# Optimization experiments

Hardware: AMD Instinct MI355X
Metric: run time of the kernel (lower is better)

## Reference

```python
import jax, jax.numpy as jnp
import numpy as np

N_HEAD = 16
ROPE_BASE = 10000.0


def _rope_cos_sin(T, D, dtype):
    # inv_freq over even dims, freqs concatenated twice (rotate_half convention)
    inv_freq = 1.0 / (ROPE_BASE ** (jnp.arange(0, D, 2, dtype=jnp.float32) / D))
    t = jnp.arange(T, dtype=jnp.float32)
    freqs = jnp.outer(t, inv_freq)          # [T, D/2]
    emb = jnp.concatenate([freqs, freqs], axis=-1)  # [T, D]
    return jnp.cos(emb).astype(dtype), jnp.sin(emb).astype(dtype)


def _rotate_half(x):
    x1, x2 = jnp.split(x, 2, axis=-1)
    return jnp.concatenate([-x2, x1], axis=-1)


def setup_inputs() -> dict:
    key = jax.random.key(0)
    ks = jax.random.split(key, 5)
    B, T, C = 2, 2048, 1024
    s = 1.0 / np.sqrt(C)
    return {
        "x": jax.random.normal(ks[0], (B, T, C), jnp.float32),
        "W_attn": jax.random.normal(ks[1], (C, 3 * C), jnp.float32) * s,
        "b_attn": jax.random.normal(ks[2], (3 * C,), jnp.float32) * 0.02,
        "W_proj": jax.random.normal(ks[3], (C, C), jnp.float32) * s,
        "b_proj": jax.random.normal(ks[4], (C,), jnp.float32) * 0.02,
    }


def reference(x, W_attn, b_attn, W_proj, b_proj):
    B, T, C = x.shape
    H = N_HEAD
    D = C // H

    # fused QKV projection
    qkv = x @ W_attn + b_attn                      # [B, T, 3C]
    q, k, v = jnp.split(qkv, 3, axis=-1)
    q = q.reshape(B, T, H, D).transpose(0, 2, 1, 3)  # [B, H, T, D]
    k = k.reshape(B, T, H, D).transpose(0, 2, 1, 3)
    v = v.reshape(B, T, H, D).transpose(0, 2, 1, 3)

    # RoPE (no past_kv: applied to full q and k)
    cos, sin = _rope_cos_sin(T, D, x.dtype)        # [T, D]
    cos = cos[None, None]                          # [1, 1, T, D]
    sin = sin[None, None]
    q = q * cos + _rotate_half(q) * sin
    k = k * cos + _rotate_half(k) * sin

    # causal SDPA (dropout_p = 0 in reference)
    scale = 1.0 / np.sqrt(D)
    scores = jnp.einsum("bhqd,bhkd->bhqk", q, k) * scale
    causal = jnp.tril(jnp.ones((T, T), dtype=bool))
    scores = jnp.where(causal, scores, jnp.finfo(scores.dtype).min)
    attn = jax.nn.softmax(scores, axis=-1)
    y = jnp.einsum("bhqk,bhkd->bhqd", attn, v)     # [B, H, T, D]

    y = y.transpose(0, 2, 1, 3).reshape(B, T, C)
    y = y @ W_proj + b_proj
    return y
```

## Files before the change

kernel.cpp:

```cpp
#include <hip/hip_runtime.h>
#include <cstdint>
#include <cstddef>

#define SEQ_T 2048
#define NHEAD 16

typedef __attribute__((ext_vector_type(8))) short short8;
typedef __attribute__((ext_vector_type(4))) float f32x4;
typedef __attribute__((ext_vector_type(16))) float f32x16;

__device__ __forceinline__ unsigned short f2bf(float f) {
  union { float f; unsigned int u; } v; v.f = f;
  return (unsigned short)((v.u + 0x7FFFu + ((v.u >> 16) & 1u)) >> 16);
}

__device__ __forceinline__ unsigned cvtpk(float lo, float hi) {
  unsigned r;
  asm("v_cvt_pk_bf16_f32 %0, %1, %2" : "=v"(r) : "v"(lo), "v"(hi));
  return r;
}

#if __has_builtin(__builtin_amdgcn_permlane32_swap)
__device__ __forceinline__ void plswap(unsigned& a, unsigned& b) {
  auto r = __builtin_amdgcn_permlane32_swap(a, b, false, false);
  a = r[0];
  b = r[1];
}
#else
__device__ __forceinline__ void plswap(unsigned& a, unsigned& b) {
  asm volatile("s_nop 1\n\tv_permlane32_swap_b32 %0, %1\n\ts_nop 1"
               : "+v"(a), "+v"(b));
}
#endif

__device__ __forceinline__ float xhalf_max(float x) {
  unsigned a = __builtin_bit_cast(unsigned, x), b = a;
  plswap(a, b);
  return fmaxf(__builtin_bit_cast(float, a), __builtin_bit_cast(float, b));
}
__device__ __forceinline__ float xhalf_add(float x) {
  unsigned a = __builtin_bit_cast(unsigned, x), b = a;
  plswap(a, b);
  return __builtin_bit_cast(float, a) + __builtin_bit_cast(float, b);
}

__device__ __forceinline__ float vmax16(const f32x16 v) {
  float a0 = fmaxf(v[0], v[8]),  a1 = fmaxf(v[1], v[9]);
  float a2 = fmaxf(v[2], v[10]), a3 = fmaxf(v[3], v[11]);
  float a4 = fmaxf(v[4], v[12]), a5 = fmaxf(v[5], v[13]);
  float a6 = fmaxf(v[6], v[14]), a7 = fmaxf(v[7], v[15]);
  float b0 = fmaxf(a0, a4), b1 = fmaxf(a1, a5);
  float b2 = fmaxf(a2, a6), b3 = fmaxf(a3, a7);
  return fmaxf(fmaxf(b0, b1), fmaxf(b2, b3));
}

__device__ __forceinline__ void gl_lds16(const void* g, void* l) {
  __builtin_amdgcn_global_load_lds(
      (__attribute__((address_space(1))) void*)(void*)g,
      (__attribute__((address_space(3))) void*)l, 16, 0, 0);
}

__global__ void k_cvt(const float* __restrict__ in, unsigned short* __restrict__ out, int n4) {
  int i = blockIdx.x * 256 + threadIdx.x;
  if (i >= n4) return;
  float4 v = ((const float4*)in)[i];
  unsigned long long pk = (unsigned long long)f2bf(v.x)
                        | ((unsigned long long)f2bf(v.y) << 16)
                        | ((unsigned long long)f2bf(v.z) << 32)
                        | ((unsigned long long)f2bf(v.w) << 48);
  ((unsigned long long*)out)[i] = pk;
}

__global__ void k_tr(const float* __restrict__ in, unsigned short* __restrict__ out, int K, int N) {
  int idx = blockIdx.x * 256 + threadIdx.x;
  int n = idx % N;
  int k0 = (idx / N) * 8;
  short8 v;
#pragma unroll
  for (int j = 0; j < 8; ++j)
    v[j] = (short)f2bf(in[(size_t)(k0 + j) * N + n]);
  *(short8*)&out[(size_t)n * K + k0] = v;
}

__global__ void k_tab(float2* __restrict__ tab) {
  int idx = blockIdx.x * 256 + threadIdx.x;
  int t = idx >> 5, i = idx & 31;
  float inv = powf(10000.0f, -(float)(2 * i) / 64.0f);
  float f = (float)t * inv;
  tab[idx] = make_float2(cosf(f), sinf(f));
}

__global__ void k_gemm_qkv(const unsigned short* __restrict__ A,
                           const unsigned short* __restrict__ Bt,
                           const float* __restrict__ bias,
                           const float2* __restrict__ cs,
                           unsigned short* __restrict__ qo,
                           unsigned short* __restrict__ ko,
                           unsigned short* __restrict__ vo) {
  __shared__ unsigned short lA[128 * 32];
  __shared__ unsigned short lB[128 * 32];
  const int K = 1024;
  const int bn = blockIdx.x, bm = blockIdx.y;
  const int tid = threadIdx.x, w = tid >> 6, l = tid & 63;
  const int lr = l & 15, lh = l >> 4;
  const int wm = w >> 1, wn = w & 1;

  f32x4 acc[4][4];
#pragma unroll
  for (int m = 0; m < 4; ++m)
#pragma unroll
    for (int n = 0; n < 4; ++n)
#pragma unroll
      for (int i = 0; i < 4; ++i) acc[m][n][i] = 0.f;

  const unsigned short* ga0 = A + (size_t)(bm * 128 + w * 16 + (l >> 2)) * K + (l & 3) * 8;
  const unsigned short* gb0 = Bt + (size_t)(bn * 128 + w * 16 + (l >> 2)) * K + (l & 3) * 8;
  unsigned short* la0 = &lA[w * 512];
  unsigned short* la1 = &lA[(w + 4) * 512];
  unsigned short* lb0 = &lB[w * 512];
  unsigned short* lb1 = &lB[(w + 4) * 512];

  for (int kt = 0; kt < K; kt += 32) {
    gl_lds16(ga0 + kt, la0);
    gl_lds16(ga0 + (size_t)64 * K + kt, la1);
    gl_lds16(gb0 + kt, lb0);
    gl_lds16(gb0 + (size_t)64 * K + kt, lb1);
    __syncthreads();
    short8 af[4], bf[4];
#pragma unroll
    for (int m = 0; m < 4; ++m) af[m] = *(const short8*)&lA[(wm * 64 + m * 16 + lr) * 32 + lh * 8];
#pragma unroll
    for (int n = 0; n < 4; ++n) bf[n] = *(const short8*)&lB[(wn * 64 + n * 16 + lr) * 32 + lh * 8];
#pragma unroll
    for (int m = 0; m < 4; ++m)
#pragma unroll
      for (int n = 0; n < 4; ++n)
        acc[m][n] = __builtin_amdgcn_mfma_f32_16x16x32_bf16(af[m], bf[n], acc[m][n], 0, 0, 0);
    __syncthreads();
  }

  const int col0 = bn * 128 + wn * 64;
  const int row0 = bm * 128 + wm * 64;
  const int sec = col0 >> 10;
  const int hh = (col0 >> 6) & 15;
  float bl[4];
#pragma unroll
  for (int n = 0; n < 4; ++n) bl[n] = bias[col0 + n * 16 + lr];

  if (sec == 2) {
    const int b = row0 >> 11;
    unsigned short* vtp = vo + (size_t)(b * 16 + hh) * 64 * 2048;
#pragma unroll
    for (int n = 0; n < 4; ++n) {
      int d = n * 16 + lr;
#pragma unroll
      for (int m = 0; m < 4; ++m) {
        int t = (row0 + m * 16 + lh * 4) & 2047;
        unsigned long long pk = (unsigned long long)f2bf(acc[m][n][0] + bl[n])
                              | ((unsigned long long)f2bf(acc[m][n][1] + bl[n]) << 16)
                              | ((unsigned long long)f2bf(acc[m][n][2] + bl[n]) << 32)
                              | ((unsigned long long)f2bf(acc[m][n][3] + bl[n]) << 48);
        *(unsigned long long*)&vtp[(size_t)d * 2048 + t] = pk;
      }
    }
  } else {
    unsigned short* dst = (sec == 0) ? qo : ko;
#pragma unroll
    for (int m = 0; m < 4; ++m)
#pragma unroll
      for (int i = 0; i < 4; ++i) {
        int row = row0 + m * 16 + lh * 4 + i;
        int t = row & 2047, b = row >> 11;
        size_t ob = ((size_t)(b * 16 + hh) * 2048 + t) * 64;
#pragma unroll
        for (int n = 0; n < 4; ++n) {
          float v = acc[m][n][i] + bl[n];
          float pv = acc[m][n ^ 2][i] + bl[n ^ 2];
          int d = n * 16 + lr;
          float2 c = cs[t * 32 + (d & 31)];
          float rot = (d < 32) ? -pv : pv;
          dst[ob + d] = f2bf(v * c.x + rot * c.y);
        }
      }
  }
}

__global__ __launch_bounds__(512, 4) void k_attn(const unsigned short* __restrict__ Q,
                       const unsigned short* __restrict__ Kg,
                       const unsigned short* __restrict__ VT,
                       unsigned short* __restrict__ O) {
  __shared__ unsigned short kl[2][128 * 64];
  __shared__ unsigned short vl[2][64 * 128];
  const int id = blockIdx.x;
  const int xcd = id & 7, u = id >> 3;
  const int g = u >> 4;
  const int bh = xcd * 4 + g;
  const int s = (u + g * 4) & 15;
  const int qt = (s & 1) ? 15 - (s >> 1) : (s >> 1);
  const int tid = threadIdx.x, w = tid >> 6, l = tid & 63;
  const int wq = w & 3, wk = w >> 2;
  const int lq = l & 31, hi = l >> 5;
  const size_t base = (size_t)bh * SEQ_T * 64;
  const float CE = 0.18033688f;
  const float DTHR = 44.3614f;

  const int qrow = qt * 128 + wq * 32 + lq;
  short8 qf[4];
#pragma unroll
  for (int c = 0; c < 4; ++c)
    qf[c] = *(const short8*)&Q[base + (size_t)qrow * 64 + c * 16 + hi * 8];

  const int kv0 = tid >> 3;
  const unsigned short* ks0 = Kg + base + (size_t)kv0 * 64 + (((tid & 7) ^ (kv0 & 7)) * 8);
  const int dv0 = tid >> 4;
  const unsigned short* vs0 = VT + base + (size_t)dv0 * 2048 + (((tid & 15) ^ (dv0 & 15)) * 8);

#define STAGE(KT, BSEL) do { \
    const unsigned short* kp_ = ks0 + (size_t)(KT) * 8192; \
    const unsigned short* vp_ = vs0 + (size_t)(KT) * 128;  \
    unsigned short* kd_ = &kl[BSEL][w * 512]; \
    unsigned short* vd_ = &vl[BSEL][w * 512]; \
    gl_lds16(kp_,         kd_);        gl_lds16(kp_ + 4096,  kd_ + 4096); \
    gl_lds16(vp_,         vd_);        gl_lds16(vp_ + 65536, vd_ + 4096); \
  } while (0)

  float mi = -1.0e30f, li = 0.f;
  f32x16 oc0, oc1;
#pragma unroll
  for (int r = 0; r < 16; ++r) { oc0[r] = 0.f; oc1[r] = 0.f; }

  const int nkt = qt + 1;
  STAGE(0, 0);
  __syncthreads();

  for (int kt = 0; kt < nkt; ++kt) {
    const int cur = kt & 1;
    if (kt + 1 < nkt) STAGE(kt + 1, cur ^ 1);
    const unsigned short* kb = &kl[cur][0];
    const unsigned short* vb = &vl[cur][0];

    f32x16 st[2];
#pragma unroll
    for (int tt = 0; tt < 2; ++tt)
#pragma unroll
      for (int r = 0; r < 16; ++r) st[tt][r] = 0.f;

    __builtin_amdgcn_s_setprio(1);
#pragma unroll
    for (int tt = 0; tt < 2; ++tt) {
      const int rowb = (wk * 64 + tt * 32 + lq) * 64;
#pragma unroll
      for (int c = 0; c < 4; ++c) {
        const short8 kf = *(const short8*)&kb[rowb + (((c * 2 + hi) ^ (lq & 7)) * 8)];
        st[tt] = __builtin_amdgcn_mfma_f32_32x32x16_bf16(kf, qf[c], st[tt], 0, 0, 0);
      }
    }
    __builtin_amdgcn_s_setprio(0);

    if (kt == nkt - 1) {
#pragma unroll
      for (int tt = 0; tt < 2; ++tt)
#pragma unroll
        for (int r = 0; r < 16; ++r) {
          int kvg = kt * 128 + wk * 64 + tt * 32 + (r & 3) + 8 * (r >> 2) + 4 * hi;
          if (kvg > qrow) st[tt][r] = -3.0e38f;
        }
    }

    float tm = xhalf_max(fmaxf(vmax16(st[0]), vmax16(st[1])));

    if (!__all(tm <= mi + DTHR)) {
      float mn = fmaxf(mi, tm);
      float scq = exp2f((mi - mn) * CE);
      mi = mn;
      li *= scq;
#pragma unroll
      for (int r = 0; r < 16; ++r) {
        float sc_r = __shfl(scq, (r & 3) + 8 * (r >> 2) + 4 * hi, 64);
        oc0[r] *= sc_r;
        oc1[r] *= sc_r;
      }
    }

    const float nb = mi * CE;
    float rs = 0.f;
#pragma unroll
    for (int tt = 0; tt < 2; ++tt)
#pragma unroll
      for (int r = 0; r < 16; ++r) {
        float p = exp2f(fmaf(st[tt][r], CE, -nb));
        st[tt][r] = p;
        rs += p;
      }
    li += xhalf_add(rs);

    short8 pa[4];
#pragma unroll
    for (int kc = 0; kc < 4; ++kc) {
      const int tt = kc >> 1, o = (kc & 1) * 8;
      unsigned w0 = cvtpk(st[tt][o + 0], st[tt][o + 1]);
      unsigned w1 = cvtpk(st[tt][o + 2], st[tt][o + 3]);
      unsigned w2 = cvtpk(st[tt][o + 4], st[tt][o + 5]);
      unsigned w3 = cvtpk(st[tt][o + 6], st[tt][o + 7]);
      plswap(w0, w2);
      plswap(w1, w3);
      uint4 F;
      F.x = w0; F.y = w1; F.z = w2; F.w = w3;
      pa[kc] = __builtin_bit_cast(short8, F);
    }

    __builtin_amdgcn_s_setprio(1);
#pragma unroll
    for (int kc = 0; kc < 4; ++kc) {
      const int chs = ((wk * 8 + kc * 2 + hi) ^ (lq & 15)) * 8;
      const short8 vb0 = *(const short8*)&vb[lq * 128 + chs];
      oc0 = __builtin_amdgcn_mfma_f32_32x32x16_bf16(pa[kc], vb0, oc0, 0, 0, 0);
      const short8 vb1 = *(const short8*)&vb[(32 + lq) * 128 + chs];
      oc1 = __builtin_amdgcn_mfma_f32_32x32x16_bf16(pa[kc], vb1, oc1, 0, 0, 0);
    }
    __builtin_amdgcn_s_setprio(0);

    if (kt + 1 < nkt) __syncthreads();
  }

  __syncthreads();
  float* obuf = (float*)&kl[0][0];
  float* mlb  = (float*)&vl[0][0];
  if (wk == 1) {
#pragma unroll
    for (int r = 0; r < 16; ++r) {
      const int q = (r & 3) + 8 * (r >> 2) + 4 * hi;
      obuf[wq * 2048 + q * 64 + lq]      = oc0[r];
      obuf[wq * 2048 + q * 64 + 32 + lq] = oc1[r];
    }
    if (hi == 0) {
      mlb[wq * 64 + lq * 2 + 0] = mi;
      mlb[wq * 64 + lq * 2 + 1] = li;
    }
  }
  __syncthreads();
  if (wk == 0) {
    const int hh = bh & 15, bb = bh >> 4;
#pragma unroll
    for (int r = 0; r < 16; ++r) {
      const int q = (r & 3) + 8 * (r >> 2) + 4 * hi;
      float m0 = __shfl(mi, q, 64), l0 = __shfl(li, q, 64);
      float m1 = mlb[wq * 64 + q * 2 + 0], l1 = mlb[wq * 64 + q * 2 + 1];
      float mm = fmaxf(m0, m1);
      float f0 = exp2f((m0 - mm) * CE), f1 = exp2f((m1 - mm) * CE);
      float inv = 1.0f / (f0 * l0 + f1 * l1);
      float o0 = (f0 * oc0[r] + f1 * obuf[wq * 2048 + q * 64 + lq]) * inv;
      float o1 = (f0 * oc1[r] + f1 * obuf[wq * 2048 + q * 64 + 32 + lq]) * inv;
      int qg = qt * 128 + wq * 32 + q;
      size_t ob = (size_t)(bb * 2048 + qg) * 1024 + hh * 64;
      O[ob + lq]      = f2bf(o0);
      O[ob + 32 + lq] = f2bf(o1);
    }
  }
#undef STAGE
}

__global__ void k_gemm_proj(const unsigned short* __restrict__ A,
                            const unsigned short* __restrict__ Bt,
                            const float* __restrict__ bias,
                            float* __restrict__ out) {
  __shared__ unsigned short lA[128 * 32];
  __shared__ unsigned short lB[128 * 32];
  const int K = 1024;
  const int bn = blockIdx.x, bm = blockIdx.y;
  const int tid = threadIdx.x, w = tid >> 6, l = tid & 63;
  const int lr = l & 15, lh = l >> 4;
  const int wm = w >> 1, wn = w & 1;

  f32x4 acc[4][4];
#pragma unroll
  for (int m = 0; m < 4; ++m)
#pragma unroll
    for (int n = 0; n < 4; ++n)
#pragma unroll
      for (int i = 0; i < 4; ++i) acc[m][n][i] = 0.f;

  const unsigned short* ga0 = A + (size_t)(bm * 128 + w * 16 + (l >> 2)) * K + (l & 3) * 8;
  const unsigned short* gb0 = Bt + (size_t)(bn * 128 + w * 16 + (l >> 2)) * K + (l & 3) * 8;
  unsigned short* la0 = &lA[w * 512];
  unsigned short* la1 = &lA[(w + 4) * 512];
  unsigned short* lb0 = &lB[w * 512];
  unsigned short* lb1 = &lB[(w + 4) * 512];

  for (int kt = 0; kt < K; kt += 32) {
    gl_lds16(ga0 + kt, la0);
    gl_lds16(ga0 + (size_t)64 * K + kt, la1);
    gl_lds16(gb0 + kt, lb0);
    gl_lds16(gb0 + (size_t)64 * K + kt, lb1);
    __syncthreads();
    short8 af[4], bf[4];
#pragma unroll
    for (int m = 0; m < 4; ++m) af[m] = *(const short8*)&lA[(wm * 64 + m * 16 + lr) * 32 + lh * 8];
#pragma unroll
    for (int n = 0; n < 4; ++n) bf[n] = *(const short8*)&lB[(wn * 64 + n * 16 + lr) * 32 + lh * 8];
#pragma unroll
    for (int m = 0; m < 4; ++m)
#pragma unroll
      for (int n = 0; n < 4; ++n)
        acc[m][n] = __builtin_amdgcn_mfma_f32_16x16x32_bf16(af[m], bf[n], acc[m][n], 0, 0, 0);
    __syncthreads();
  }

  const int col0 = bn * 128 + wn * 64;
  const int row0 = bm * 128 + wm * 64;
  float bl[4];
#pragma unroll
  for (int n = 0; n < 4; ++n) bl[n] = bias[col0 + n * 16 + lr];
#pragma unroll
  for (int m = 0; m < 4; ++m)
#pragma unroll
    for (int i = 0; i < 4; ++i) {
      int row = row0 + m * 16 + lh * 4 + i;
#pragma unroll
      for (int n = 0; n < 4; ++n)
        out[(size_t)row * 1024 + col0 + n * 16 + lr] = acc[m][n][i] + bl[n];
    }
}

extern "C" void kernel_launch(void* const* d_in, const int* in_sizes, int n_in,
                              void* d_out, int out_size, void* d_ws, size_t ws_size,
                              hipStream_t stream) {
  const float* x     = (const float*)d_in[0];
  const float* Wattn = (const float*)d_in[1];
  const float* battn = (const float*)d_in[2];
  const float* Wproj = (const float*)d_in[3];
  const float* bproj = (const float*)d_in[4];
  float* out = (float*)d_out;

  char* ws = (char*)d_ws;
  unsigned short* xb  = (unsigned short*)(ws);
  unsigned short* wat = (unsigned short*)(ws + (8ull  << 20));
  unsigned short* wpt = (unsigned short*)(ws + (14ull << 20));
  unsigned short* qa  = (unsigned short*)(ws + (16ull << 20));
  unsigned short* ka  = (unsigned short*)(ws + (24ull << 20));
  unsigned short* va  = (unsigned short*)(ws + (32ull << 20));
  unsigned short* ob  = (unsigned short*)(ws + (40ull << 20));
  float2* cs          = (float2*)(ws + (48ull << 20));

  k_cvt<<<(4096 * 1024 / 4) / 256, 256, 0, stream>>>(x, xb, 4096 * 1024 / 4);
  k_tr<<<(3072 * 1024 / 8) / 256, 256, 0, stream>>>(Wattn, wat, 1024, 3072);
  k_tr<<<(1024 * 1024 / 8) / 256, 256, 0, stream>>>(Wproj, wpt, 1024, 1024);
  k_tab<<<(2048 * 32) / 256, 256, 0, stream>>>(cs);
  k_gemm_qkv<<<dim3(24, 32), 256, 0, stream>>>(xb, wat, battn, cs, qa, ka, va);
  k_attn<<<512, 512, 0, stream>>>(qa, ka, va, ob);
  k_gemm_proj<<<dim3(8, 32), 256, 0, stream>>>(ob, wpt, bproj, out);
}
```

Measured before the change: 138.8 us.

## Merge prep kernels and software-pipeline attention with 64-wide KV tiles

Folds the four preparation kernels (x conversion, two weight transposes, RoPE table) into a single launch with block-range dispatch, which removes three kernel launch gaps. The attention kernel moves from 128-wide double-buffered KV tiles to 64-wide triple-buffered tiles. QK^T for the next tile is computed before the softmax and PV of the current tile, so MFMA work overlaps with the exp and reduction work. The smaller tiles halve LDS use but double the number of loop iterations and barriers.

```diff
diff --git a/kernel.cpp b/kernel.cpp
--- a/kernel.cpp
+++ b/kernel.cpp
@@ -60,34 +60,45 @@
       (__attribute__((address_space(3))) void*)l, 16, 0, 0);
 }
 
-__global__ void k_cvt(const float* __restrict__ in, unsigned short* __restrict__ out, int n4) {
-  int i = blockIdx.x * 256 + threadIdx.x;
-  if (i >= n4) return;
-  float4 v = ((const float4*)in)[i];
-  unsigned long long pk = (unsigned long long)f2bf(v.x)
-                        | ((unsigned long long)f2bf(v.y) << 16)
-                        | ((unsigned long long)f2bf(v.z) << 32)
-                        | ((unsigned long long)f2bf(v.w) << 48);
-  ((unsigned long long*)out)[i] = pk;
-}
-
-__global__ void k_tr(const float* __restrict__ in, unsigned short* __restrict__ out, int K, int N) {
-  int idx = blockIdx.x * 256 + threadIdx.x;
-  int n = idx % N;
-  int k0 = (idx / N) * 8;
-  short8 v;
-#pragma unroll
-  for (int j = 0; j < 8; ++j)
-    v[j] = (short)f2bf(in[(size_t)(k0 + j) * N + n]);
-  *(short8*)&out[(size_t)n * K + k0] = v;
-}
-
-__global__ void k_tab(float2* __restrict__ tab) {
-  int idx = blockIdx.x * 256 + threadIdx.x;
-  int t = idx >> 5, i = idx & 31;
-  float inv = powf(10000.0f, -(float)(2 * i) / 64.0f);
-  float f = (float)t * inv;
-  tab[idx] = make_float2(cosf(f), sinf(f));
+__global__ void k_prep(const float* __restrict__ x,
+                       const float* __restrict__ Wa,
+                       const float* __restrict__ Wp,
+                       unsigned short* __restrict__ xb,
+                       unsigned short* __restrict__ wat,
+                       unsigned short* __restrict__ wpt,
+                       float2* __restrict__ tab) {
+  const int b = blockIdx.x, tid = threadIdx.x;
+  if (b < 4096) {
+    int i = b * 256 + tid;
+    float4 v = ((const float4*)x)[i];
+    unsigned long long pk = (unsigned long long)f2bf(v.x)
+                          | ((unsigned long long)f2bf(v.y) << 16)
+                          | ((unsigned long long)f2bf(v.z) << 32)
+                          | ((unsigned long long)f2bf(v.w) << 48);
+    ((unsigned long long*)xb)[i] = pk;
+  } else if (b < 5632) {
+    int idx = (b - 4096) * 256 + tid;
+    int n = idx % 3072, k0 = (idx / 3072) * 8;
+    short8 v;
+#pragma unroll
+    for (int j = 0; j < 8; ++j)
+      v[j] = (short)f2bf(Wa[(size_t)(k0 + j) * 3072 + n]);
+    *(short8*)&wat[(size_t)n * 1024 + k0] = v;
+  } else if (b < 6144) {
+    int idx = (b - 5632) * 256 + tid;
+    int n = idx & 1023, k0 = (idx >> 10) * 8;
+    short8 v;
+#pragma unroll
+    for (int j = 0; j < 8; ++j)
+      v[j] = (short)f2bf(Wp[(size_t)(k0 + j) * 1024 + n]);
+    *(short8*)&wpt[(size_t)n * 1024 + k0] = v;
+  } else {
+    int idx = (b - 6144) * 256 + tid;
+    int t = idx >> 5, i = idx & 31;
+    float inv = powf(10000.0f, -(float)(2 * i) / 64.0f);
+    float f = (float)t * inv;
+    tab[idx] = make_float2(cosf(f), sinf(f));
+  }
 }
 
 __global__ void k_gemm_qkv(const unsigned short* __restrict__ A,
@@ -189,8 +200,8 @@
                        const unsigned short* __restrict__ Kg,
                        const unsigned short* __restrict__ VT,
                        unsigned short* __restrict__ O) {
-  __shared__ unsigned short kl[2][128 * 64];
-  __shared__ unsigned short vl[2][64 * 128];
+  __shared__ unsigned short kl[3][64 * 64];
+  __shared__ unsigned short vl[3][64 * 64];
   const int id = blockIdx.x;
   const int xcd = id & 7, u = id >> 3;
   const int g = u >> 4;
@@ -210,65 +221,53 @@
   for (int c = 0; c < 4; ++c)
     qf[c] = *(const short8*)&Q[base + (size_t)qrow * 64 + c * 16 + hi * 8];
 
-  const int kv0 = tid >> 3;
-  const unsigned short* ks0 = Kg + base + (size_t)kv0 * 64 + (((tid & 7) ^ (kv0 & 7)) * 8);
-  const int dv0 = tid >> 4;
-  const unsigned short* vs0 = VT + base + (size_t)dv0 * 2048 + (((tid & 15) ^ (dv0 & 15)) * 8);
-
-#define STAGE(KT, BSEL) do { \
-    const unsigned short* kp_ = ks0 + (size_t)(KT) * 8192; \
-    const unsigned short* vp_ = vs0 + (size_t)(KT) * 128;  \
-    unsigned short* kd_ = &kl[BSEL][w * 512]; \
-    unsigned short* vd_ = &vl[BSEL][w * 512]; \
-    gl_lds16(kp_,         kd_);        gl_lds16(kp_ + 4096,  kd_ + 4096); \
-    gl_lds16(vp_,         vd_);        gl_lds16(vp_ + 65536, vd_ + 4096); \
+  const int r0 = tid >> 3, c8 = tid & 7;
+  const unsigned short* ks0 = Kg + base + (size_t)r0 * 64 + ((c8 ^ (r0 & 7)) * 8);
+  const unsigned short* vs0 = VT + base + (size_t)r0 * 2048 + ((c8 ^ (r0 & 7)) * 8);
+
+#define STAGE(KT, B) do { \
+    gl_lds16(ks0 + (size_t)(KT) * 4096, &kl[B][w * 512]); \
+    gl_lds16(vs0 + (size_t)(KT) * 64,   &vl[B][w * 512]); \
   } while (0)
 
+#define QKSTEP(KB, ST) do { \
+    const unsigned short* kb_ = &kl[KB][0]; \
+    _Pragma("unroll") \
+    for (int c_ = 0; c_ < 4; ++c_) { \
+      const short8 kf_ = *(const short8*)&kb_[(wk * 32 + lq) * 64 + (((2 * c_ + hi) ^ (lq & 7)) * 8)]; \
+      ST = __builtin_amdgcn_mfma_f32_32x32x16_bf16(kf_, qf[c_], ST, 0, 0, 0); \
+    } \
+  } while (0)
+
   float mi = -1.0e30f, li = 0.f;
-  f32x16 oc0, oc1;
-#pragma unroll
-  for (int r = 0; r < 16; ++r) { oc0[r] = 0.f; oc1[r] = 0.f; }
-
-  const int nkt = qt + 1;
+  f32x16 oc0, oc1, stC, stN;
+#pragma unroll
+  for (int r = 0; r < 16; ++r) { oc0[r] = 0.f; oc1[r] = 0.f; stC[r] = 0.f; }
+
+  const int nkt = 2 * qt + 2;
   STAGE(0, 0);
+  STAGE(1, 1);
   __syncthreads();
+  QKSTEP(0, stC);
 
   for (int kt = 0; kt < nkt; ++kt) {
-    const int cur = kt & 1;
-    if (kt + 1 < nkt) STAGE(kt + 1, cur ^ 1);
-    const unsigned short* kb = &kl[cur][0];
-    const unsigned short* vb = &vl[cur][0];
-
-    f32x16 st[2];
-#pragma unroll
-    for (int tt = 0; tt < 2; ++tt)
-#pragma unroll
-      for (int r = 0; r < 16; ++r) st[tt][r] = 0.f;
-
-    __builtin_amdgcn_s_setprio(1);
-#pragma unroll
-    for (int tt = 0; tt < 2; ++tt) {
-      const int rowb = (wk * 64 + tt * 32 + lq) * 64;
-#pragma unroll
-      for (int c = 0; c < 4; ++c) {
-        const short8 kf = *(const short8*)&kb[rowb + (((c * 2 + hi) ^ (lq & 7)) * 8)];
-        st[tt] = __builtin_amdgcn_mfma_f32_32x32x16_bf16(kf, qf[c], st[tt], 0, 0, 0);
+    if (kt + 2 < nkt) STAGE(kt + 2, (kt + 2) % 3);
+
+    if (kt + 1 < nkt) {
+#pragma unroll
+      for (int r = 0; r < 16; ++r) stN[r] = 0.f;
+      QKSTEP((kt + 1) % 3, stN);
+    }
+
+    if (kt >= nkt - 2) {
+#pragma unroll
+      for (int r = 0; r < 16; ++r) {
+        int kvg = kt * 64 + wk * 32 + (r & 3) + 8 * (r >> 2) + 4 * hi;
+        if (kvg > qrow) stC[r] = -3.0e38f;
       }
     }
-    __builtin_amdgcn_s_setprio(0);
-
-    if (kt == nkt - 1) {
-#pragma unroll
-      for (int tt = 0; tt < 2; ++tt)
-#pragma unroll
-        for (int r = 0; r < 16; ++r) {
-          int kvg = kt * 128 + wk * 64 + tt * 32 + (r & 3) + 8 * (r >> 2) + 4 * hi;
-          if (kvg > qrow) st[tt][r] = -3.0e38f;
-        }
-    }
-
-    float tm = xhalf_max(fmaxf(vmax16(st[0]), vmax16(st[1])));
-
+
+    float tm = xhalf_max(vmax16(stC));
     if (!__all(tm <= mi + DTHR)) {
       float mn = fmaxf(mi, tm);
       float scq = exp2f((mi - mn) * CE);
@@ -281,27 +280,24 @@
         oc1[r] *= sc_r;
       }
     }
-
     const float nb = mi * CE;
     float rs = 0.f;
 #pragma unroll
-    for (int tt = 0; tt < 2; ++tt)
-#pragma unroll
-      for (int r = 0; r < 16; ++r) {
-        float p = exp2f(fmaf(st[tt][r], CE, -nb));
-        st[tt][r] = p;
-        rs += p;
-      }
+    for (int r = 0; r < 16; ++r) {
+      float p = exp2f(fmaf(stC[r], CE, -nb));
+      stC[r] = p;
+      rs += p;
+    }
     li += xhalf_add(rs);
 
-    short8 pa[4];
-#pragma unroll
-    for (int kc = 0; kc < 4; ++kc) {
-      const int tt = kc >> 1, o = (kc & 1) * 8;
-      unsigned w0 = cvtpk(st[tt][o + 0], st[tt][o + 1]);
-      unsigned w1 = cvtpk(st[tt][o + 2], st[tt][o + 3]);
-      unsigned w2 = cvtpk(st[tt][o + 4], st[tt][o + 5]);
-      unsigned w3 = cvtpk(st[tt][o + 6], st[tt][o + 7]);
+    short8 pa[2];
+#pragma unroll
+    for (int kc = 0; kc < 2; ++kc) {
+      const int o = kc * 8;
+      unsigned w0 = cvtpk(stC[o + 0], stC[o + 1]);
+      unsigned w1 = cvtpk(stC[o + 2], stC[o + 3]);
+      unsigned w2 = cvtpk(stC[o + 4], stC[o + 5]);
+      unsigned w3 = cvtpk(stC[o + 6], stC[o + 7]);
       plswap(w0, w2);
       plswap(w1, w3);
       uint4 F;
@@ -309,23 +305,31 @@
       pa[kc] = __builtin_bit_cast(short8, F);
     }
 
-    __builtin_amdgcn_s_setprio(1);
-#pragma unroll
-    for (int kc = 0; kc < 4; ++kc) {
-      const int chs = ((wk * 8 + kc * 2 + hi) ^ (lq & 15)) * 8;
-      const short8 vb0 = *(const short8*)&vb[lq * 128 + chs];
-      oc0 = __builtin_amdgcn_mfma_f32_32x32x16_bf16(pa[kc], vb0, oc0, 0, 0, 0);
-      const short8 vb1 = *(const short8*)&vb[(32 + lq) * 128 + chs];
-      oc1 = __builtin_amdgcn_mfma_f32_32x32x16_bf16(pa[kc], vb1, oc1, 0, 0, 0);
-    }
-    __builtin_amdgcn_s_setprio(0);
-
+    {
+      const unsigned short* vb_ = &vl[kt % 3][0];
+      short8 vbf[2][2];
+#pragma unroll
+      for (int dt = 0; dt < 2; ++dt)
+#pragma unroll
+        for (int kc = 0; kc < 2; ++kc)
+          vbf[dt][kc] = *(const short8*)&vb_[(dt * 32 + lq) * 64 +
+                          (((wk * 4 + kc * 2 + hi) ^ (lq & 7)) * 8)];
+      __builtin_amdgcn_s_setprio(1);
+#pragma unroll
+      for (int kc = 0; kc < 2; ++kc) {
+        oc0 = __builtin_amdgcn_mfma_f32_32x32x16_bf16(pa[kc], vbf[0][kc], oc0, 0, 0, 0);
+        oc1 = __builtin_amdgcn_mfma_f32_32x32x16_bf16(pa[kc], vbf[1][kc], oc1, 0, 0, 0);
+      }
+      __builtin_amdgcn_s_setprio(0);
+    }
+
+    stC = stN;
     if (kt + 1 < nkt) __syncthreads();
   }
 
   __syncthreads();
   float* obuf = (float*)&kl[0][0];
-  float* mlb  = (float*)&vl[0][0];
+  float* mlb  = (float*)&vl[2][0];
   if (wk == 1) {
 #pragma unroll
     for (int r = 0; r < 16; ++r) {
@@ -358,6 +362,7 @@
     }
   }
 #undef STAGE
+#undef QKSTEP
 }
 
 __global__ void k_gemm_proj(const unsigned short* __restrict__ A,
@@ -442,10 +447,7 @@
   unsigned short* ob  = (unsigned short*)(ws + (40ull << 20));
   float2* cs          = (float2*)(ws + (48ull << 20));
 
-  k_cvt<<<(4096 * 1024 / 4) / 256, 256, 0, stream>>>(x, xb, 4096 * 1024 / 4);
-  k_tr<<<(3072 * 1024 / 8) / 256, 256, 0, stream>>>(Wattn, wat, 1024, 3072);
-  k_tr<<<(1024 * 1024 / 8) / 256, 256, 0, stream>>>(Wproj, wpt, 1024, 1024);
-  k_tab<<<(2048 * 32) / 256, 256, 0, stream>>>(cs);
+  k_prep<<<6400, 256, 0, stream>>>(x, Wattn, Wproj, xb, wat, wpt, cs);
   k_gemm_qkv<<<dim3(24, 32), 256, 0, stream>>>(xb, wat, battn, cs, qa, ka, va);
   k_attn<<<512, 512, 0, stream>>>(qa, ka, va, ob);
   k_gemm_proj<<<dim3(8, 32), 256, 0, stream>>>(ob, wpt, bproj, out);
```

Result: no change. 140.2 us (+1.0%).
